# Kernel optimization log

Measured on AMD Instinct MI355X. Metric: run time of the kernel, lower is better.

The kernel has to match this reference:

```python
import jax, jax.numpy as jnp
import numpy as np

B, T, D, H = 4, 2048, 1024, 16
DH = D // H

def setup_inputs() -> dict:
    key = jax.random.key(0)
    ks = jax.random.split(key, 8)
    scale = 1.0 / np.sqrt(D)
    return {
        "q": jax.random.normal(ks[0], (B, T, D), dtype=jnp.float32),
        "k": jax.random.normal(ks[1], (B, T, D), dtype=jnp.float32),
        "v": jax.random.normal(ks[2], (B, T, D), dtype=jnp.float32),
        "wq": jax.random.normal(ks[3], (D, D), dtype=jnp.float32) * scale,
        "wk": jax.random.normal(ks[4], (D, D), dtype=jnp.float32) * scale,
        "wv": jax.random.normal(ks[5], (D, D), dtype=jnp.float32) * scale,
        "wo": jax.random.normal(ks[6], (D, D), dtype=jnp.float32) * scale,
        "mask": jnp.tril(jnp.ones((T, T), dtype=bool)),  # causal [Tq,Tk]
    }

def reference(q, k, v, wq, wk, wv, wo, mask):
    Bq, Tq, C = q.shape
    Tk = k.shape[1]
    # nn.Linear(bias=False): y = x @ W.T, W is [out,in]
    qh = (q @ wq.T).reshape(Bq, Tq, H, DH).transpose(0, 2, 1, 3)  # [B,H,Tq,DH]
    kh = (k @ wk.T).reshape(Bq, Tk, H, DH).transpose(0, 2, 1, 3)
    vh = (v @ wv.T).reshape(Bq, Tk, H, DH).transpose(0, 2, 1, 3)
    att = jnp.einsum("bhqd,bhkd->bhqk", qh, kh) / np.sqrt(DH)
    att = jnp.where(mask[None, None, :, :], att, -jnp.inf)
    att = jax.nn.softmax(att, axis=-1)
    out = jnp.einsum("bhqk,bhkd->bhqd", att, vh)
    out = out.transpose(0, 2, 1, 3).reshape(Bq, Tq, C)
    return out @ wo.T
```

## Files before the change

kernel.cpp:

```cpp
#include <hip/hip_runtime.h>
#include <hip/hip_bf16.h>

typedef short bf16x8 __attribute__((ext_vector_type(8)));
typedef float f32x4 __attribute__((ext_vector_type(4)));
typedef float f32x16 __attribute__((ext_vector_type(16)));

#define N_B 4
#define N_T 2048
#define N_D 1024
#define N_H 16
#define N_DH 64

#define Q_SCALE 0.18033688011112042f

__device__ __forceinline__ unsigned short f2bf(float f) {
  union { float f; unsigned int u; } c; c.f = f;
  unsigned int u = c.u;
  return (unsigned short)((u + 0x7FFFu + ((u >> 16) & 1u)) >> 16);
}

__device__ __forceinline__ unsigned cvtpk_bf16(float lo, float hi) {
  unsigned r;
  asm("v_cvt_pk_bf16_f32 %0, %1, %2" : "=v"(r) : "v"(lo), "v"(hi));
  return r;
}

__device__ __forceinline__ void gll16(const unsigned short* g, unsigned short* l) {
  __builtin_amdgcn_global_load_lds(
      (const __attribute__((address_space(1))) unsigned int*)(const void*)g,
      (__attribute__((address_space(3))) unsigned int*)(void*)l, 16, 0, 0);
}

__global__ void cast_all(const float* __restrict__ wq, const float* __restrict__ wk,
                         const float* __restrict__ wv, const float* __restrict__ wo,
                         const float* __restrict__ q, const float* __restrict__ k,
                         const float* __restrict__ v,
                         unsigned short* __restrict__ ws) {
  const int z = blockIdx.z;
  const float* srcs[7] = {wq, wk, wv, wo, q, k, v};
  const int size = (z < 4) ? (N_D * N_D) : (N_B * N_T * N_D);
  const size_t off = (z < 4) ? (size_t)z * (N_D * N_D)
                             : (size_t)4 * (N_D * N_D) + (size_t)(z - 4) * (N_B * N_T * N_D);
  const int i = (blockIdx.x * 256 + threadIdx.x) * 8;
  if (i >= size) return;
  const float* src = srcs[z];
  float4 a = *(const float4*)(src + i);
  float4 b = *(const float4*)(src + i + 4);
  bf16x8 p;
  p[0] = (short)f2bf(a.x); p[1] = (short)f2bf(a.y);
  p[2] = (short)f2bf(a.z); p[3] = (short)f2bf(a.w);
  p[4] = (short)f2bf(b.x); p[5] = (short)f2bf(b.y);
  p[6] = (short)f2bf(b.z); p[7] = (short)f2bf(b.w);
  *(bf16x8*)(ws + off + i) = p;
}

__launch_bounds__(256, 2)
__global__ void proj_qkv(const unsigned short* __restrict__ qb,
                         const unsigned short* __restrict__ kb,
                         const unsigned short* __restrict__ vb,
                         const unsigned short* __restrict__ wq,
                         const unsigned short* __restrict__ wk,
                         const unsigned short* __restrict__ wv,
                         unsigned short* __restrict__ qh,
                         unsigned short* __restrict__ kh,
                         unsigned short* __restrict__ vt) {
  const int z = blockIdx.z;
  const unsigned short* X = (z == 0) ? qb : (z == 1) ? kb : vb;
  const unsigned short* W = (z == 0) ? wq : (z == 1) ? wk : wv;
  unsigned short* O = (z == 0) ? qh : (z == 1) ? kh : vt;

  __shared__ unsigned short lds_a[128 * 64];
  __shared__ unsigned short lds_b[128 * 64];

  const int tid = threadIdx.x;
  const int wave = tid >> 6, lane = tid & 63;
  const int wm = wave >> 1, wn = wave & 1;
  const int lr = lane & 15, lg = lane >> 4;
  const int orig = blockIdx.y * 8 + blockIdx.x;
  const int swz = (orig & 7) * 64 + (orig >> 3);
  const int m0 = (swz >> 3) * 128, n0 = (swz & 7) * 128;
  const int sw = (lr & 7) << 4;

  f32x4 acc[4][4] = {};

  for (int k0 = 0; k0 < N_D; k0 += 64) {
    __syncthreads();
#pragma unroll
    for (int it = 0; it < 4; ++it) {
      int c = it * 256 + tid;
      int row = c >> 3;
      int sb = ((c & 7) * 16) ^ ((row & 7) << 4);
      gll16(&X[(size_t)(m0 + row) * N_D + k0 + (sb >> 1)], &lds_a[c * 8]);
      gll16(&W[(size_t)(n0 + row) * N_D + k0 + (sb >> 1)], &lds_b[c * 8]);
    }
    __syncthreads();

#pragma unroll
    for (int kk = 0; kk < 2; ++kk) {
      bf16x8 af[4], bfr[4];
      const int cb = (lg * 16 + kk * 64);
#pragma unroll
      for (int m = 0; m < 4; ++m)
        af[m] = *(bf16x8*)&lds_a[(wm * 64 + m * 16 + lr) * 64 + ((cb ^ sw) >> 1)];
#pragma unroll
      for (int n = 0; n < 4; ++n)
        bfr[n] = *(bf16x8*)&lds_b[(wn * 64 + n * 16 + lr) * 64 + ((cb ^ sw) >> 1)];
#pragma unroll
      for (int m = 0; m < 4; ++m)
#pragma unroll
        for (int n = 0; n < 4; ++n)
          acc[m][n] = __builtin_amdgcn_mfma_f32_16x16x32_bf16(af[m], bfr[n], acc[m][n], 0, 0, 0);
    }
  }

  const float osc = (z == 0) ? Q_SCALE : 1.0f;
#pragma unroll
  for (int m = 0; m < 4; ++m)
#pragma unroll
    for (int n = 0; n < 4; ++n)
#pragma unroll
      for (int r = 0; r < 4; ++r) {
        int row = m0 + wm * 64 + m * 16 + lg * 4 + r;
        int col = n0 + wn * 64 + n * 16 + lr;
        int b = row >> 11, t = row & (N_T - 1);
        int hh = col >> 6, dh = col & 63;
        unsigned short val = f2bf(acc[m][n][r] * osc);
        if (z < 2)
          O[(((size_t)(b * N_H + hh)) * N_T + t) * N_DH + dh] = val;
        else
          O[(((size_t)(b * N_H + hh)) * N_DH + dh) * N_T + t] = val;
      }
}

__launch_bounds__(256, 2)
__global__ void proj_out(const unsigned short* __restrict__ A,
                         const unsigned short* __restrict__ W,
                         float* __restrict__ out) {
  __shared__ unsigned short lds_a[128 * 64];
  __shared__ unsigned short lds_b[128 * 64];

  const int tid = threadIdx.x;
  const int wave = tid >> 6, lane = tid & 63;
  const int wm = wave >> 1, wn = wave & 1;
  const int lr = lane & 15, lg = lane >> 4;
  const int orig = blockIdx.y * 8 + blockIdx.x;
  const int swz = (orig & 7) * 64 + (orig >> 3);
  const int m0 = (swz >> 3) * 128, n0 = (swz & 7) * 128;
  const int sw = (lr & 7) << 4;

  f32x4 acc[4][4] = {};

  for (int k0 = 0; k0 < N_D; k0 += 64) {
    __syncthreads();
#pragma unroll
    for (int it = 0; it < 4; ++it) {
      int c = it * 256 + tid;
      int row = c >> 3;
      int sb = ((c & 7) * 16) ^ ((row & 7) << 4);
      gll16(&A[(size_t)(m0 + row) * N_D + k0 + (sb >> 1)], &lds_a[c * 8]);
      gll16(&W[(size_t)(n0 + row) * N_D + k0 + (sb >> 1)], &lds_b[c * 8]);
    }
    __syncthreads();

#pragma unroll
    for (int kk = 0; kk < 2; ++kk) {
      bf16x8 af[4], bfr[4];
      const int cb = (lg * 16 + kk * 64);
#pragma unroll
      for (int m = 0; m < 4; ++m)
        af[m] = *(bf16x8*)&lds_a[(wm * 64 + m * 16 + lr) * 64 + ((cb ^ sw) >> 1)];
#pragma unroll
      for (int n = 0; n < 4; ++n)
        bfr[n] = *(bf16x8*)&lds_b[(wn * 64 + n * 16 + lr) * 64 + ((cb ^ sw) >> 1)];
#pragma unroll
      for (int m = 0; m < 4; ++m)
#pragma unroll
        for (int n = 0; n < 4; ++n)
          acc[m][n] = __builtin_amdgcn_mfma_f32_16x16x32_bf16(af[m], bfr[n], acc[m][n], 0, 0, 0);
    }
  }

#pragma unroll
  for (int m = 0; m < 4; ++m)
#pragma unroll
    for (int n = 0; n < 4; ++n)
#pragma unroll
      for (int r = 0; r < 4; ++r) {
        int row = m0 + wm * 64 + m * 16 + lg * 4 + r;
        int col = n0 + wn * 64 + n * 16 + lr;
        out[(size_t)row * N_D + col] = acc[m][n][r];
      }
}

__launch_bounds__(256, 2)
__global__ void attn(const unsigned short* __restrict__ qh,
                     const unsigned short* __restrict__ kh,
                     const unsigned short* __restrict__ vt,
                     unsigned short* __restrict__ att) {
  __shared__ unsigned short k_lds[2][64 * 64];
  __shared__ unsigned short v_lds[2][64 * 64];

  const int tid = threadIdx.x;
  const int wave = tid >> 6, lane = tid & 63;
  const int l31 = lane & 31, hi = lane >> 5;
  const int bh = blockIdx.y;
  const size_t base = (size_t)bh * N_T * N_DH;
  const unsigned short* Q = qh + base;
  const unsigned short* K = kh + base;
  const unsigned short* V = vt + base;
  const int b = bh >> 4, h = bh & 15;
  const int swr = (l31 & 7) << 4;

  auto stage = [&](int buf, int kb2) {
    const int kk0 = kb2 * 64;
#pragma unroll
    for (int it = 0; it < 2; ++it) {
      int c = it * 256 + tid;
      int row = c >> 3;
      int sb = ((c & 7) * 16) ^ ((row & 7) << 4);
      gll16(&K[(size_t)(kk0 + row) * N_DH + (sb >> 1)], &k_lds[buf][c * 8]);
      gll16(&V[(size_t)row * N_T + kk0 + (sb >> 1)], &v_lds[buf][c * 8]);
    }
  };

  for (int half = 0; half < 2; ++half) {
    const int qt = half ? (15 - (int)blockIdx.x) : (int)blockIdx.x;
    const int q0 = qt * 128;
    const int q0w = q0 + wave * 32;

    bf16x8 qf[4];
#pragma unroll
    for (int i = 0; i < 4; ++i)
      qf[i] = *(const bf16x8*)&Q[(size_t)(q0w + l31) * N_DH + i * 16 + hi * 8];

    float m_r = -INFINITY, l_lane = 0.f;
    f32x16 o0 = {}, o1 = {};

    const int nkb = 2 * qt + 2;

    __syncthreads();
    stage(0, 0);

    for (int kb = 0; kb < nkb; ++kb) {
      const int cur = kb & 1;
      __syncthreads();
      if (kb + 1 < nkb) stage(cur ^ 1, kb + 1);

      const unsigned short* kt_ = k_lds[cur];
      const unsigned short* vt_ = v_lds[cur];

#pragma unroll
      for (int ks = 0; ks < 2; ++ks) {
        const int kgb = kb * 64 + ks * 32;
        if (kgb > q0w + 31) continue;

        f32x16 s = {};
#pragma unroll
        for (int i = 0; i < 4; ++i) {
          bf16x8 kf = *(const bf16x8*)&kt_[(ks * 32 + l31) * 64 +
                                           (((i * 32 + hi * 16) ^ swr) >> 1)];
          s = __builtin_amdgcn_mfma_f32_32x32x16_bf16(kf, qf[i], s, 0, 0, 0);
        }

        if (kgb == q0w) {
#pragma unroll
          for (int j = 0; j < 16; ++j)
            if ((j & 3) + 8 * (j >> 2) + 4 * hi > l31) s[j] = -1e30f;
        }

        float mx = s[0];
#pragma unroll
        for (int j = 1; j < 16; ++j) mx = fmaxf(mx, s[j]);
        mx = fmaxf(mx, __shfl_xor(mx, 32));
        if (__any(mx > m_r + 8.0f)) {
          float mn = fmaxf(m_r, mx);
          float al = exp2f(m_r - mn);
          m_r = mn;
          l_lane *= al;
#pragma unroll
          for (int j = 0; j < 16; ++j) {
            float aj = __shfl(al, (j & 3) + 8 * (j >> 2) + 4 * hi);
            o0[j] *= aj; o1[j] *= aj;
          }
        }

#pragma unroll
        for (int j = 0; j < 16; ++j) s[j] = exp2f(s[j] - m_r);
        float lsum = 0.f;
#pragma unroll
        for (int j = 0; j < 16; ++j) lsum += s[j];
        l_lane += lsum + __shfl_xor(lsum, 32);

        unsigned t01 = cvtpk_bf16(s[0], s[1]),   t45 = cvtpk_bf16(s[4], s[5]);
        unsigned t23 = cvtpk_bf16(s[2], s[3]),   t67 = cvtpk_bf16(s[6], s[7]);
        unsigned u01 = cvtpk_bf16(s[8], s[9]),   u45 = cvtpk_bf16(s[12], s[13]);
        unsigned u23 = cvtpk_bf16(s[10], s[11]), u67 = cvtpk_bf16(s[14], s[15]);
        unsigned x01 = __shfl_xor(t01, 32), x45 = __shfl_xor(t45, 32);
        unsigned x23 = __shfl_xor(t23, 32), x67 = __shfl_xor(t67, 32);
        unsigned y01 = __shfl_xor(u01, 32), y45 = __shfl_xor(u45, 32);
        unsigned y23 = __shfl_xor(u23, 32), y67 = __shfl_xor(u67, 32);
        union { unsigned u[4]; bf16x8 v; } pa0, pa1;
        pa0.u[0] = hi ? x45 : t01;  pa0.u[1] = hi ? x67 : t23;
        pa0.u[2] = hi ? t45 : x01;  pa0.u[3] = hi ? t67 : x23;
        pa1.u[0] = hi ? y45 : u01;  pa1.u[1] = hi ? y67 : u23;
        pa1.u[2] = hi ? u45 : y01;  pa1.u[3] = hi ? u67 : y23;

        const int c0 = ((ks * 64 + hi * 16) ^ swr) >> 1;
        const int c1 = ((ks * 64 + 32 + hi * 16) ^ swr) >> 1;
        bf16x8 v00 = *(const bf16x8*)&vt_[l31 * 64 + c0];
        bf16x8 v01 = *(const bf16x8*)&vt_[(32 + l31) * 64 + c0];
        bf16x8 v10 = *(const bf16x8*)&vt_[l31 * 64 + c1];
        bf16x8 v11 = *(const bf16x8*)&vt_[(32 + l31) * 64 + c1];

        o0 = __builtin_amdgcn_mfma_f32_32x32x16_bf16(pa0.v, v00, o0, 0, 0, 0);
        o1 = __builtin_amdgcn_mfma_f32_32x32x16_bf16(pa0.v, v01, o1, 0, 0, 0);
        o0 = __builtin_amdgcn_mfma_f32_32x32x16_bf16(pa1.v, v10, o0, 0, 0, 0);
        o1 = __builtin_amdgcn_mfma_f32_32x32x16_bf16(pa1.v, v11, o1, 0, 0, 0);
      }
    }

#pragma unroll
    for (int j = 0; j < 16; ++j) {
      int ridx = (j & 3) + 8 * (j >> 2) + 4 * hi;
      float inv = 1.0f / __shfl(l_lane, ridx);
      int t = q0w + ridx;
      size_t rowb = ((size_t)(b * N_T + t)) * N_D + h * 64 + l31;
      att[rowb]      = f2bf(o0[j] * inv);
      att[rowb + 32] = f2bf(o1[j] * inv);
    }
  }
}

extern "C" void kernel_launch(void* const* d_in, const int* in_sizes, int n_in,
                              void* d_out, int out_size, void* d_ws, size_t ws_size,
                              hipStream_t stream) {
  (void)in_sizes; (void)n_in; (void)out_size; (void)ws_size;
  const float* q  = (const float*)d_in[0];
  const float* k  = (const float*)d_in[1];
  const float* v  = (const float*)d_in[2];
  const float* wq = (const float*)d_in[3];
  const float* wk = (const float*)d_in[4];
  const float* wv = (const float*)d_in[5];
  const float* wo = (const float*)d_in[6];
  float* out = (float*)d_out;

  unsigned short* ws = (unsigned short*)d_ws;
  const size_t W_ELEMS = (size_t)N_D * N_D;
  const size_t T_ELEMS = (size_t)N_B * N_T * N_D;
  unsigned short* wqb = ws;
  unsigned short* wkb = wqb + W_ELEMS;
  unsigned short* wvb = wkb + W_ELEMS;
  unsigned short* wob = wvb + W_ELEMS;
  unsigned short* qb  = wob + W_ELEMS;
  unsigned short* kb  = qb + T_ELEMS;
  unsigned short* vb  = kb + T_ELEMS;
  unsigned short* qhb = vb + T_ELEMS;
  unsigned short* khb = qhb + T_ELEMS;
  unsigned short* vtb = khb + T_ELEMS;
  unsigned short* att = qb;

  cast_all<<<dim3(4096, 1, 7), 256, 0, stream>>>(wq, wk, wv, wo, q, k, v, ws);
  proj_qkv<<<dim3(8, 64, 3), 256, 0, stream>>>(qb, kb, vb, wqb, wkb, wvb, qhb, khb, vtb);
  attn<<<dim3(8, N_B * N_H), 256, 0, stream>>>(qhb, khb, vtb, att);
  proj_out<<<dim3(8, 64), 256, 0, stream>>>(att, wob, out);
}
```

Measured before the change: 209.7 us.

## Fuse activation bf16 cast into QKV projection and compute softmax sums via MFMA

The separate cast pass over the q/k/v activations is removed. The projection kernel now stages fp32 activation tiles straight into LDS and converts them to bf16 on the fly, which avoids writing and re-reading the bf16 copies. In attention, the row-sum of the softmax is accumulated by an extra MFMA against a ones vector instead of VALU adds and shuffles, and s_setprio is set around the MFMA blocks. In exchange, the projection kernel uses twice the LDS for its A tile, which may reduce occupancy, and each attention step issues two more MFMAs.

After: 200.2 us. 1.05x faster.

```diff
diff --git a/kernel.cpp b/kernel.cpp
--- a/kernel.cpp
+++ b/kernel.cpp
@@ -30,20 +30,20 @@
       (const __attribute__((address_space(1))) unsigned int*)(const void*)g,
       (__attribute__((address_space(3))) unsigned int*)(void*)l, 16, 0, 0);
 }
-
-__global__ void cast_all(const float* __restrict__ wq, const float* __restrict__ wk,
-                         const float* __restrict__ wv, const float* __restrict__ wo,
-                         const float* __restrict__ q, const float* __restrict__ k,
-                         const float* __restrict__ v,
-                         unsigned short* __restrict__ ws) {
+__device__ __forceinline__ void gll16f(const float* g, float* l) {
+  __builtin_amdgcn_global_load_lds(
+      (const __attribute__((address_space(1))) unsigned int*)(const void*)g,
+      (__attribute__((address_space(3))) unsigned int*)(void*)l, 16, 0, 0);
+}
+
+__global__ void cast_w(const float* __restrict__ wq, const float* __restrict__ wk,
+                       const float* __restrict__ wv, const float* __restrict__ wo,
+                       unsigned short* __restrict__ ws) {
   const int z = blockIdx.z;
-  const float* srcs[7] = {wq, wk, wv, wo, q, k, v};
-  const int size = (z < 4) ? (N_D * N_D) : (N_B * N_T * N_D);
-  const size_t off = (z < 4) ? (size_t)z * (N_D * N_D)
-                             : (size_t)4 * (N_D * N_D) + (size_t)(z - 4) * (N_B * N_T * N_D);
+  const float* srcs[4] = {wq, wk, wv, wo};
+  const float* src = srcs[z];
+  unsigned short* d = ws + (size_t)z * (N_D * N_D);
   const int i = (blockIdx.x * 256 + threadIdx.x) * 8;
-  if (i >= size) return;
-  const float* src = srcs[z];
   float4 a = *(const float4*)(src + i);
   float4 b = *(const float4*)(src + i + 4);
   bf16x8 p;
@@ -51,13 +51,13 @@
   p[2] = (short)f2bf(a.z); p[3] = (short)f2bf(a.w);
   p[4] = (short)f2bf(b.x); p[5] = (short)f2bf(b.y);
   p[6] = (short)f2bf(b.z); p[7] = (short)f2bf(b.w);
-  *(bf16x8*)(ws + off + i) = p;
+  *(bf16x8*)(d + i) = p;
 }
 
 __launch_bounds__(256, 2)
-__global__ void proj_qkv(const unsigned short* __restrict__ qb,
-                         const unsigned short* __restrict__ kb,
-                         const unsigned short* __restrict__ vb,
+__global__ void proj_qkv(const float* __restrict__ qf32,
+                         const float* __restrict__ kf32,
+                         const float* __restrict__ vf32,
                          const unsigned short* __restrict__ wq,
                          const unsigned short* __restrict__ wk,
                          const unsigned short* __restrict__ wv,
@@ -65,11 +65,11 @@
                          unsigned short* __restrict__ kh,
                          unsigned short* __restrict__ vt) {
   const int z = blockIdx.z;
-  const unsigned short* X = (z == 0) ? qb : (z == 1) ? kb : vb;
+  const float* X = (z == 0) ? qf32 : (z == 1) ? kf32 : vf32;
   const unsigned short* W = (z == 0) ? wq : (z == 1) ? wk : wv;
   unsigned short* O = (z == 0) ? qh : (z == 1) ? kh : vt;
 
-  __shared__ unsigned short lds_a[128 * 64];
+  __shared__ float lds_af[128 * 64];
   __shared__ unsigned short lds_b[128 * 64];
 
   const int tid = threadIdx.x;
@@ -86,11 +86,17 @@
   for (int k0 = 0; k0 < N_D; k0 += 64) {
     __syncthreads();
 #pragma unroll
+    for (int it = 0; it < 8; ++it) {
+      int c = it * 256 + tid;
+      int row = c >> 4;
+      int sb = ((c & 15) * 16) ^ ((row & 7) << 4);
+      gll16f(&X[(size_t)(m0 + row) * N_D + k0 + (sb >> 2)], &lds_af[c * 4]);
+    }
+#pragma unroll
     for (int it = 0; it < 4; ++it) {
       int c = it * 256 + tid;
       int row = c >> 3;
       int sb = ((c & 7) * 16) ^ ((row & 7) << 4);
-      gll16(&X[(size_t)(m0 + row) * N_D + k0 + (sb >> 1)], &lds_a[c * 8]);
       gll16(&W[(size_t)(n0 + row) * N_D + k0 + (sb >> 1)], &lds_b[c * 8]);
     }
     __syncthreads();
@@ -98,13 +104,21 @@
 #pragma unroll
     for (int kk = 0; kk < 2; ++kk) {
       bf16x8 af[4], bfr[4];
-      const int cb = (lg * 16 + kk * 64);
-#pragma unroll
-      for (int m = 0; m < 4; ++m)
-        af[m] = *(bf16x8*)&lds_a[(wm * 64 + m * 16 + lr) * 64 + ((cb ^ sw) >> 1)];
+#pragma unroll
+      for (int m = 0; m < 4; ++m) {
+        const char* pbase = (const char*)&lds_af[(wm * 64 + m * 16 + lr) * 64];
+        const int cb = (kk * 128 + lg * 32) ^ sw;
+        float4 f0 = *(const float4*)(pbase + cb);
+        float4 f1 = *(const float4*)(pbase + (cb ^ 16));
+        union { unsigned u[4]; bf16x8 v; } pk;
+        pk.u[0] = cvtpk_bf16(f0.x, f0.y); pk.u[1] = cvtpk_bf16(f0.z, f0.w);
+        pk.u[2] = cvtpk_bf16(f1.x, f1.y); pk.u[3] = cvtpk_bf16(f1.z, f1.w);
+        af[m] = pk.v;
+      }
+      const int cb2 = (lg * 16 + kk * 64);
 #pragma unroll
       for (int n = 0; n < 4; ++n)
-        bfr[n] = *(bf16x8*)&lds_b[(wn * 64 + n * 16 + lr) * 64 + ((cb ^ sw) >> 1)];
+        bfr[n] = *(bf16x8*)&lds_b[(wn * 64 + n * 16 + lr) * 64 + ((cb2 ^ sw) >> 1)];
 #pragma unroll
       for (int m = 0; m < 4; ++m)
 #pragma unroll
@@ -211,6 +225,10 @@
   const int b = bh >> 4, h = bh & 15;
   const int swr = (l31 & 7) << 4;
 
+  bf16x8 ones;
+#pragma unroll
+  for (int j = 0; j < 8; ++j) ones[j] = (short)0x3F80;
+
   auto stage = [&](int buf, int kb2) {
     const int kk0 = kb2 * 64;
 #pragma unroll
@@ -233,7 +251,8 @@
     for (int i = 0; i < 4; ++i)
       qf[i] = *(const bf16x8*)&Q[(size_t)(q0w + l31) * N_DH + i * 16 + hi * 8];
 
-    float m_r = -INFINITY, l_lane = 0.f;
+    float m_r = -INFINITY;
+    f32x16 l_acc = {};
     f32x16 o0 = {}, o1 = {};
 
     const int nkb = 2 * qt + 2;
@@ -255,12 +274,14 @@
         if (kgb > q0w + 31) continue;
 
         f32x16 s = {};
+        __builtin_amdgcn_s_setprio(1);
 #pragma unroll
         for (int i = 0; i < 4; ++i) {
           bf16x8 kf = *(const bf16x8*)&kt_[(ks * 32 + l31) * 64 +
                                            (((i * 32 + hi * 16) ^ swr) >> 1)];
           s = __builtin_amdgcn_mfma_f32_32x32x16_bf16(kf, qf[i], s, 0, 0, 0);
         }
+        __builtin_amdgcn_s_setprio(0);
 
         if (kgb == q0w) {
 #pragma unroll
@@ -276,20 +297,15 @@
           float mn = fmaxf(m_r, mx);
           float al = exp2f(m_r - mn);
           m_r = mn;
-          l_lane *= al;
 #pragma unroll
           for (int j = 0; j < 16; ++j) {
             float aj = __shfl(al, (j & 3) + 8 * (j >> 2) + 4 * hi);
-            o0[j] *= aj; o1[j] *= aj;
+            o0[j] *= aj; o1[j] *= aj; l_acc[j] *= aj;
           }
         }
 
 #pragma unroll
         for (int j = 0; j < 16; ++j) s[j] = exp2f(s[j] - m_r);
-        float lsum = 0.f;
-#pragma unroll
-        for (int j = 0; j < 16; ++j) lsum += s[j];
-        l_lane += lsum + __shfl_xor(lsum, 32);
 
         unsigned t01 = cvtpk_bf16(s[0], s[1]),   t45 = cvtpk_bf16(s[4], s[5]);
         unsigned t23 = cvtpk_bf16(s[2], s[3]),   t67 = cvtpk_bf16(s[6], s[7]);
@@ -312,18 +328,21 @@
         bf16x8 v10 = *(const bf16x8*)&vt_[l31 * 64 + c1];
         bf16x8 v11 = *(const bf16x8*)&vt_[(32 + l31) * 64 + c1];
 
+        __builtin_amdgcn_s_setprio(1);
         o0 = __builtin_amdgcn_mfma_f32_32x32x16_bf16(pa0.v, v00, o0, 0, 0, 0);
         o1 = __builtin_amdgcn_mfma_f32_32x32x16_bf16(pa0.v, v01, o1, 0, 0, 0);
         o0 = __builtin_amdgcn_mfma_f32_32x32x16_bf16(pa1.v, v10, o0, 0, 0, 0);
         o1 = __builtin_amdgcn_mfma_f32_32x32x16_bf16(pa1.v, v11, o1, 0, 0, 0);
+        l_acc = __builtin_amdgcn_mfma_f32_32x32x16_bf16(pa0.v, ones, l_acc, 0, 0, 0);
+        l_acc = __builtin_amdgcn_mfma_f32_32x32x16_bf16(pa1.v, ones, l_acc, 0, 0, 0);
+        __builtin_amdgcn_s_setprio(0);
       }
     }
 
 #pragma unroll
     for (int j = 0; j < 16; ++j) {
-      int ridx = (j & 3) + 8 * (j >> 2) + 4 * hi;
-      float inv = 1.0f / __shfl(l_lane, ridx);
-      int t = q0w + ridx;
+      float inv = 1.0f / l_acc[j];
+      int t = q0w + (j & 3) + 8 * (j >> 2) + 4 * hi;
       size_t rowb = ((size_t)(b * N_T + t)) * N_D + h * 64 + l31;
       att[rowb]      = f2bf(o0[j] * inv);
       att[rowb + 32] = f2bf(o1[j] * inv);
@@ -351,16 +370,13 @@
   unsigned short* wkb = wqb + W_ELEMS;
   unsigned short* wvb = wkb + W_ELEMS;
   unsigned short* wob = wvb + W_ELEMS;
-  unsigned short* qb  = wob + W_ELEMS;
-  unsigned short* kb  = qb + T_ELEMS;
-  unsigned short* vb  = kb + T_ELEMS;
-  unsigned short* qhb = vb + T_ELEMS;
+  unsigned short* qhb = wob + W_ELEMS;
   unsigned short* khb = qhb + T_ELEMS;
   unsigned short* vtb = khb + T_ELEMS;
-  unsigned short* att = qb;
-
-  cast_all<<<dim3(4096, 1, 7), 256, 0, stream>>>(wq, wk, wv, wo, q, k, v, ws);
-  proj_qkv<<<dim3(8, 64, 3), 256, 0, stream>>>(qb, kb, vb, wqb, wkb, wvb, qhb, khb, vtb);
+  unsigned short* att = vtb + T_ELEMS;
+
+  cast_w<<<dim3(512, 1, 4), 256, 0, stream>>>(wq, wk, wv, wo, ws);
+  proj_qkv<<<dim3(8, 64, 3), 256, 0, stream>>>(q, k, v, wqb, wkb, wvb, qhb, khb, vtb);
   attn<<<dim3(8, N_B * N_H), 256, 0, stream>>>(qhb, khb, vtb, att);
   proj_out<<<dim3(8, 64), 256, 0, stream>>>(att, wob, out);
 }
```
